# Kernel tuning notes

Hardware: AMD Instinct MI355X
Metric: run time of the kernel (lower is better)

The kernel has to match this reference:

```python
import jax, jax.numpy as jnp
import numpy as np

B, S, D = 1, 2048, 2048
HQ, HKV = 32, 8
HD = D // HQ          # 64
G = HQ // HKV         # 4 query heads per kv head


def apply_rope(x, freq):
    # x: (b, h, s, hd); freq: (s, hd//2) angles. Llama-style pairwise rotation.
    cos = jnp.cos(freq)  # (s, hd//2)
    sin = jnp.sin(freq)
    xr = x.reshape(*x.shape[:-1], HD // 2, 2)
    xe, xo = xr[..., 0], xr[..., 1]
    re = xe * cos - xo * sin
    ro = xe * sin + xo * cos
    return jnp.stack([re, ro], axis=-1).reshape(x.shape)


def setup_inputs() -> dict:
    key = jax.random.key(0)
    k1, k2, k3, k4, k5 = jax.random.split(key, 5)
    x = jax.random.normal(k1, (B, S, D), dtype=jnp.float32)
    # RoPE angles: pos * inv_freq, theta=10000
    inv_freq = 1.0 / (10000.0 ** (jnp.arange(0, HD, 2, dtype=jnp.float32) / HD))
    freq = jnp.arange(S, dtype=jnp.float32)[:, None] * inv_freq[None, :]  # (S, HD//2)
    mask = jnp.tril(jnp.ones((S, S), dtype=jnp.int32))
    scale = D ** -0.5
    wq = jax.random.normal(k2, (D, HQ * HD), dtype=jnp.float32) * scale
    wk = jax.random.normal(k3, (D, HKV * HD), dtype=jnp.float32) * scale
    wv = jax.random.normal(k4, (D, HKV * HD), dtype=jnp.float32) * scale
    wo = jax.random.normal(k5, (HQ * HD, D), dtype=jnp.float32) * scale
    return {"x": x, "freq": freq, "mask": mask, "wq": wq, "wk": wk, "wv": wv, "wo": wo}


def reference(x, freq, mask, wq, wk, wv, wo):
    b, s, d = x.shape
    q = (x @ wq).reshape(b, s, HQ, HD).transpose(0, 2, 1, 3)    # (b,HQ,s,hd)
    k = (x @ wk).reshape(b, s, HKV, HD).transpose(0, 2, 1, 3)   # (b,HKV,s,hd)
    v = (x @ wv).reshape(b, s, HKV, HD).transpose(0, 2, 1, 3)
    q = apply_rope(q, freq[:s])
    k = apply_rope(k, freq[:s])
    # GQA: broadcast kv heads over groups instead of repeat_interleave
    qg = q.reshape(b, HKV, G, s, HD)
    scores = jnp.einsum('bhgsd,bhtd->bhgst', qg, k)             # (b,HKV,G,s,s)
    scores = jnp.where(mask[:s, :s] == 0, -jnp.inf, scores)
    w = jax.nn.softmax(scores * (HD ** -0.5), axis=-1)
    out = jnp.einsum('bhgst,bhtd->bhgsd', w, v)
    out = out.reshape(b, HQ, s, HD).transpose(0, 2, 1, 3).reshape(b, s, HQ * HD)
    return out @ wo
```

## Files before the change

kernel.cpp:

```cpp
#include <hip/hip_runtime.h>

typedef unsigned short u16;
typedef unsigned int u32;
typedef unsigned long long u64;

using bf16x8 = __bf16 __attribute__((ext_vector_type(8)));
using f32x4  = float  __attribute__((ext_vector_type(4)));

#define LDS_SPACE __attribute__((address_space(3)))
#define GLB_SPACE __attribute__((address_space(1)))

static __device__ __forceinline__ u16 f2bf(float f) {
  union { float f; u32 u; } c; c.f = f;
  u32 u = c.u;
  return (u16)((u + 0x7fffu + ((u >> 16) & 1u)) >> 16);
}
static __device__ __forceinline__ float bf2f(u16 u) {
  union { u32 u; float f; } c; c.u = ((u32)u) << 16;
  return c.f;
}

static __device__ __forceinline__ void fence_barrier() {
  asm volatile("" ::: "memory");
  __builtin_amdgcn_s_barrier();
  asm volatile("" ::: "memory");
}

constexpr float SC = 0.18033688011112042f;

__device__ __constant__ unsigned char kItems[40] = {
  12, 28, 29, 42, 44, 45, 46, 57, 59, 60, 61, 62, 63,
  24, 25, 37, 38, 40, 41, 49, 51, 52, 53, 54, 55, 56, 58,
  8, 20, 21, 32, 33, 34, 36, 48, 50,
  16, 17,
  4,
  0
};

__global__ __launch_bounds__(256) void prep_k(const float* __restrict__ x,
                                              const float* __restrict__ wq,
                                              const float* __restrict__ wk,
                                              const float* __restrict__ wv,
                                              const float* __restrict__ wo,
                                              u16* __restrict__ x_bf,
                                              u16* __restrict__ wqkv_t,
                                              u16* __restrict__ wo_t) {
  const int b = blockIdx.x;
  if (b < 4096) {
    int i = b * 256 + threadIdx.x;
    float4 v = ((const float4*)x)[i];
    ushort4 o;
    o.x = f2bf(v.x); o.y = f2bf(v.y); o.z = f2bf(v.z); o.w = f2bf(v.w);
    ((ushort4*)x_bf)[i] = o;
    return;
  }
  const float* src; u16* dst; int C, bx, by; float scale = 1.0f;
  if (b < 8192)      { src = wq; dst = wqkv_t; C = 2048; int t = b - 4096; bx = t & 63; by = t >> 6; scale = SC; }
  else if (b < 9216) { src = wk; dst = wqkv_t + (size_t)2048 * 2048; C = 512; int t = b - 8192; bx = t & 15; by = t >> 4; }
  else if (b < 10240){ src = wv; dst = wqkv_t + (size_t)2560 * 2048; C = 512; int t = b - 9216; bx = t & 15; by = t >> 4; }
  else               { src = wo; dst = wo_t; C = 2048; int t = b - 10240; bx = t & 63; by = t >> 6; }
  __shared__ float t[32][33];
  const int lx = threadIdx.x & 31, ly = threadIdx.x >> 5;
  const int r0 = by * 32, c0 = bx * 32;
  #pragma unroll
  for (int i = 0; i < 32; i += 8)
    t[ly + i][lx] = src[(size_t)(r0 + ly + i) * C + c0 + lx];
  __syncthreads();
  #pragma unroll
  for (int i = 0; i < 32; i += 8)
    dst[(size_t)(c0 + ly + i) * 2048 + r0 + lx] = f2bf(t[lx][ly + i] * scale);
}

__global__ __launch_bounds__(256) void vtrans_k(const u16* __restrict__ Y,
                                                u16* __restrict__ Vt) {
  __shared__ u16 t[64][72];
  const int s0 = blockIdx.x * 64;
  const int c0 = blockIdx.y * 64;
  const int lx = threadIdx.x & 63, ly = threadIdx.x >> 6;
  #pragma unroll
  for (int i = 0; i < 64; i += 4)
    t[i + ly][lx] = Y[(size_t)(s0 + i + ly) * 3072 + 2560 + c0 + lx];
  __syncthreads();
  #pragma unroll
  for (int i = 0; i < 64; i += 4)
    Vt[(size_t)(c0 + i + ly) * 2048 + s0 + lx] = t[lx][i + ly];
}

template <typename OutT, int BN>
__global__ __launch_bounds__(256) void gemm64_k(const u16* __restrict__ A,
                                                const u16* __restrict__ Bt,
                                                OutT* __restrict__ C,
                                                int M, int N, int K) {
  constexpr int WN = BN / 32;
  __shared__ u16 As[2][64 * 64];
  __shared__ u16 Bs[2][BN * 64];
  const int tid = threadIdx.x, lane = tid & 63, w = tid >> 6;
  const int wr = w >> 1, wc = w & 1;
  const int bm = blockIdx.y, bn = blockIdx.x;
  const int l15 = lane & 15, lq = lane >> 4;
  f32x4 acc[2][WN] = {};

  const int srow8 = lane >> 3;
  const int scolb = ((lane & 7) ^ srow8) * 16;
  const u16* AgR = A + (size_t)(bm * 64 + w * 16 + srow8) * K;
  const u16* BgR = Bt + (size_t)(bn * BN + w * (BN / 4) + srow8) * K;

  auto stage = [&](int buf, int k0) {
    #pragma unroll
    for (int i = 0; i < 2; ++i)
      __builtin_amdgcn_global_load_lds(
          (const GLB_SPACE u32*)((const char*)(AgR + (size_t)i * 8 * K + k0) + scolb),
          (LDS_SPACE u32*)&As[buf][(w * 16 + i * 8) * 64], 16, 0, 0);
    #pragma unroll
    for (int i = 0; i < WN; ++i)
      __builtin_amdgcn_global_load_lds(
          (const GLB_SPACE u32*)((const char*)(BgR + (size_t)i * 8 * K + k0) + scolb),
          (LDS_SPACE u32*)&Bs[buf][(w * (BN / 4) + i * 8) * 64], 16, 0, 0);
  };

  stage(0, 0);
  asm volatile("s_waitcnt vmcnt(0)" ::: "memory");
  fence_barrier();

  for (int k0 = 0; k0 < K; k0 += 64) {
    const int p = (k0 >> 6) & 1;
    if (k0 + 64 < K) stage(p ^ 1, k0 + 64);

    #pragma unroll
    for (int kk = 0; kk < 2; ++kk) {
      bf16x8 a[2], b[WN];
      #pragma unroll
      for (int m = 0; m < 2; ++m) {
        const int ra = wr * 32 + m * 16 + l15;
        a[m] = *(const bf16x8*)&As[p][ra * 64 + (((kk * 4 + lq) ^ (ra & 7)) << 3)];
      }
      #pragma unroll
      for (int n = 0; n < WN; ++n) {
        const int rb = wc * (BN / 2) + n * 16 + l15;
        b[n] = *(const bf16x8*)&Bs[p][rb * 64 + (((kk * 4 + lq) ^ (rb & 7)) << 3)];
      }
      #pragma unroll
      for (int m = 0; m < 2; ++m)
        #pragma unroll
        for (int n = 0; n < WN; ++n)
          acc[m][n] = __builtin_amdgcn_mfma_f32_16x16x32_bf16(a[m], b[n], acc[m][n], 0, 0, 0);
    }

    asm volatile("s_waitcnt vmcnt(0)" ::: "memory");
    fence_barrier();
  }

  const int r0 = bm * 64 + wr * 32 + lq * 4;
  const int c0 = bn * BN + wc * (BN / 2) + l15;
  #pragma unroll
  for (int m = 0; m < 2; ++m)
    #pragma unroll
    for (int n = 0; n < WN; ++n)
      #pragma unroll
      for (int r = 0; r < 4; ++r) {
        float v = acc[m][n][r];
        size_t off = (size_t)(r0 + m * 16 + r) * N + (c0 + n * 16);
        if constexpr (sizeof(OutT) == 2) ((u16*)C)[off] = f2bf(v);
        else C[off] = v;
      }
}

__global__ __launch_bounds__(256) void rope_k(u16* __restrict__ Y,
                                              const float* __restrict__ freq) {
  int idx = blockIdx.x * 256 + threadIdx.x;
  int s = idx / 1280;
  int rem = idx - s * 1280;
  int h = rem >> 5;
  int i = rem & 31;
  int col = (h < 32) ? (h * 64 + 2 * i) : (2048 + (h - 32) * 64 + 2 * i);
  float ang = freq[s * 32 + i];
  float sn, cs;
  sincosf(ang, &sn, &cs);
  size_t base = (size_t)s * 3072 + col;
  float e = bf2f(Y[base]), o = bf2f(Y[base + 1]);
  Y[base]     = f2bf(e * cs - o * sn);
  Y[base + 1] = f2bf(e * sn + o * cs);
}

__global__ __launch_bounds__(256, 3) void attn_part_k(const u16* __restrict__ Y,
                                                      const u16* __restrict__ Vtg,
                                                      u16* __restrict__ Opart,
                                                      float2* __restrict__ Ml,
                                                      u16* __restrict__ Out) {
  __shared__ u16 Ks[2][64 * 64];
  __shared__ u16 Vs[2][64 * 64];
  __shared__ u32 Ps[4][16 * 32];
  const int w = threadIdx.x >> 6, lane = threadIdx.x & 63;
  const int l15 = lane & 15, lq = lane >> 4;

  const int b = (int)blockIdx.x;
  const int head = b & 31;
  const int idx = b >> 5;
  const int v = kItems[idx];
  const int qt = v >> 2, ch = v & 3;
  const int kvh = head >> 2;
  const int ntiles = 2 * qt + 2;
  const int nch = qt < 4 ? 1 : qt < 8 ? 2 : qt < 12 ? 3 : 4;
  const int tstart = (ch * ntiles) / nch;
  const int tend = ((ch + 1) * ntiles) / nch;
  const int q0w = qt * 128 + w * 32;

  const int srow = lane >> 3;
  const int scolb = ((lane & 7) ^ srow) * 16;
  const char* gkB = (const char*)(Y + (size_t)(w * 16 + srow) * 3072 + 2048 + kvh * 64) + scolb;
  const char* gvB = (const char*)(Vtg + (size_t)(kvh * 64 + w * 16 + srow) * 2048) + scolb;

  auto stage = [&](int buf, int t) {
    const size_t t0 = (size_t)t * 64;
    #pragma unroll
    for (int i = 0; i < 2; ++i) {
      __builtin_amdgcn_global_load_lds((const GLB_SPACE u32*)(gkB + t0 * 6144 + (size_t)i * 49152),
                                       (LDS_SPACE u32*)&Ks[buf][(w * 16 + i * 8) * 64], 16, 0, 0);
      __builtin_amdgcn_global_load_lds((const GLB_SPACE u32*)(gvB + t0 * 2 + (size_t)i * 32768),
                                       (LDS_SPACE u32*)&Vs[buf][(w * 16 + i * 8) * 64], 16, 0, 0);
    }
  };

  int rowB[4], xk[2], pwr[4], prd[2];
  #pragma unroll
  for (int kt = 0; kt < 4; ++kt) rowB[kt] = (kt * 16 + l15) * 128;
  #pragma unroll
  for (int kk = 0; kk < 2; ++kk) xk[kk] = (((kk * 4 + lq) ^ (l15 & 7)) << 4);
  #pragma unroll
  for (int n = 0; n < 4; ++n)
    pwr[n] = (l15 * 32 + ((lq * 2 + n * 8) ^ ((l15 & 7) << 2))) * 4;
  #pragma unroll
  for (int c = 0; c < 2; ++c)
    prd[c] = l15 * 128 + (((c * 32 + lq * 8) ^ ((l15 & 7) << 3)) << 1);

  bf16x8 qf[2][2];
  #pragma unroll
  for (int qs = 0; qs < 2; ++qs)
    #pragma unroll
    for (int kk = 0; kk < 2; ++kk)
      qf[qs][kk] = *(const bf16x8*)&Y[(size_t)(q0w + qs * 16 + l15) * 3072 +
                                      head * 64 + kk * 32 + lq * 8];

  float m_[2] = { -1e30f, -1e30f };
  float l_[2] = { 0.f, 0.f };
  f32x4 accO[2][4] = {};

  stage(0, tstart);
  asm volatile("s_waitcnt vmcnt(0)" ::: "memory");
  fence_barrier();

  for (int t = tstart; t < tend; ++t) {
    const int p = (t - tstart) & 1;
    stage(p ^ 1, (t + 1 < tend) ? t + 1 : t);

    const int t0 = t * 64;
    if (t0 <= q0w + 31) {
      const char* KbC = (const char*)Ks[p];
      const char* VbC = (const char*)Vs[p];

      f32x4 sc[2][4] = {};
      #pragma unroll
      for (int kk = 0; kk < 2; ++kk)
        #pragma unroll
        for (int kt = 0; kt < 4; ++kt) {
          bf16x8 a = *(const bf16x8*)(KbC + rowB[kt] + xk[kk]);
          sc[0][kt] = __builtin_amdgcn_mfma_f32_16x16x32_bf16(a, qf[0][kk], sc[0][kt], 0, 0, 0);
          sc[1][kt] = __builtin_amdgcn_mfma_f32_16x16x32_bf16(a, qf[1][kk], sc[1][kt], 0, 0, 0);
        }

      bf16x8 vf[2][4];
      #pragma unroll
      for (int c = 0; c < 2; ++c)
        #pragma unroll
        for (int dt = 0; dt < 4; ++dt)
          vf[c][dt] = *(const bf16x8*)(VbC + rowB[dt] + xk[c]);

      #pragma unroll
      for (int qs = 0; qs < 2; ++qs) {
        const int qsmin = q0w + qs * 16;
        if (t0 > qsmin + 15) continue;
        const int qrow = qsmin + l15;
        if (t0 + 63 > qsmin) {
          #pragma unroll
          for (int n = 0; n < 4; ++n)
            #pragma unroll
            for (int rr = 0; rr < 4; ++rr)
              if (t0 + n * 16 + lq * 4 + rr > qrow) sc[qs][n][rr] = -1e30f;
        }
        float a0 = fmaxf(fmaxf(sc[qs][0][0], sc[qs][0][1]), fmaxf(sc[qs][0][2], sc[qs][0][3]));
        float a1 = fmaxf(fmaxf(sc[qs][1][0], sc[qs][1][1]), fmaxf(sc[qs][1][2], sc[qs][1][3]));
        float a2 = fmaxf(fmaxf(sc[qs][2][0], sc[qs][2][1]), fmaxf(sc[qs][2][2], sc[qs][2][3]));
        float a3 = fmaxf(fmaxf(sc[qs][3][0], sc[qs][3][1]), fmaxf(sc[qs][3][2], sc[qs][3][3]));
        float mx = fmaxf(fmaxf(a0, a1), fmaxf(a2, a3));

        if (__any(mx > m_[qs] + 7.25f)) {
          float mf = mx;
          mf = fmaxf(mf, __shfl_xor(mf, 16));
          mf = fmaxf(mf, __shfl_xor(mf, 32));
          const float mnew = fmaxf(m_[qs], mf);
          const float alpha = exp2f(m_[qs] - mnew);
          l_[qs] *= alpha;
          #pragma unroll
          for (int dt = 0; dt < 4; ++dt) accO[qs][dt] *= alpha;
          m_[qs] = mnew;
        }
        const float mS = m_[qs];
        float s0 = 0.f, s1 = 0.f, s2 = 0.f, s3 = 0.f;
        char* psB = (char*)Ps[w];
        #pragma unroll
        for (int n = 0; n < 4; ++n) {
          float p0 = exp2f(sc[qs][n][0] - mS);
          float p1 = exp2f(sc[qs][n][1] - mS);
          float p2 = exp2f(sc[qs][n][2] - mS);
          float p3 = exp2f(sc[qs][n][3] - mS);
          s0 += p0; s1 += p1; s2 += p2; s3 += p3;
          u32 w0, w1;
          asm("v_cvt_pk_bf16_f32 %0, %1, %2" : "=v"(w0) : "v"(p0), "v"(p1));
          asm("v_cvt_pk_bf16_f32 %0, %1, %2" : "=v"(w1) : "v"(p2), "v"(p3));
          *(u64*)(psB + pwr[n]) = (u64)w0 | ((u64)w1 << 32);
        }
        l_[qs] += (s0 + s1) + (s2 + s3);

        #pragma unroll
        for (int c = 0; c < 2; ++c) {
          bf16x8 bb = *(const bf16x8*)(psB + prd[c]);
          #pragma unroll
          for (int dt = 0; dt < 4; ++dt)
            accO[qs][dt] = __builtin_amdgcn_mfma_f32_16x16x32_bf16(vf[c][dt], bb, accO[qs][dt], 0, 0, 0);
        }
      }
    }

    asm volatile("s_waitcnt vmcnt(0)" ::: "memory");
    fence_barrier();
  }

  if (nch == 1) {
    #pragma unroll
    for (int qs = 0; qs < 2; ++qs) {
      float lt = l_[qs];
      lt += __shfl_xor(lt, 16);
      lt += __shfl_xor(lt, 32);
      const float rl = 1.0f / lt;
      const int qrow = q0w + qs * 16 + l15;
      #pragma unroll
      for (int dt = 0; dt < 4; ++dt) {
        ushort4 o;
        o.x = f2bf(accO[qs][dt][0] * rl);
        o.y = f2bf(accO[qs][dt][1] * rl);
        o.z = f2bf(accO[qs][dt][2] * rl);
        o.w = f2bf(accO[qs][dt][3] * rl);
        *(ushort4*)&Out[(size_t)qrow * 2048 + head * 64 + dt * 16 + lq * 4] = o;
      }
    }
    return;
  }

  const int off = qt < 8 ? (qt - 4) * 2 : qt < 12 ? 8 + (qt - 8) * 3 : 20 + (qt - 12) * 4;
  const int slot = head * 36 + off + ch;
  u16* ob = Opart + (size_t)slot * 8192;
  #pragma unroll
  for (int qs = 0; qs < 2; ++qs) {
    float lt = l_[qs];
    lt += __shfl_xor(lt, 16);
    lt += __shfl_xor(lt, 32);
    const int row = w * 32 + qs * 16 + l15;
    #pragma unroll
    for (int dt = 0; dt < 4; ++dt) {
      ushort4 o;
      o.x = f2bf(accO[qs][dt][0]);
      o.y = f2bf(accO[qs][dt][1]);
      o.z = f2bf(accO[qs][dt][2]);
      o.w = f2bf(accO[qs][dt][3]);
      *(ushort4*)&ob[row * 64 + dt * 16 + lq * 4] = o;
    }
    if (lq == 0) Ml[(size_t)slot * 128 + row] = make_float2(m_[qs], lt);
  }
}

__global__ __launch_bounds__(256) void attn_comb_k(const u16* __restrict__ Opart,
                                                   const float2* __restrict__ Ml,
                                                   u16* __restrict__ Out) {
  const int b = blockIdx.x;
  const int rg = b & 3;
  const int hq = b >> 2;
  const int head = hq / 12;
  const int qt = (hq - head * 12) + 4;
  const int nch = qt < 8 ? 2 : qt < 12 ? 3 : 4;
  const int off = qt < 8 ? (qt - 4) * 2 : qt < 12 ? 8 + (qt - 8) * 3 : 20 + (qt - 12) * 4;
  const int slot0 = head * 36 + off;
  const int rl = threadIdx.x >> 3;
  const int d8 = (threadIdx.x & 7) * 8;
  const int row = rg * 32 + rl;

  float gm = -1e30f;
  #pragma unroll 4
  for (int c = 0; c < nch; ++c)
    gm = fmaxf(gm, Ml[(size_t)(slot0 + c) * 128 + row].x);
  float den = 0.f;
  float num[8] = {};
  #pragma unroll 4
  for (int c = 0; c < nch; ++c) {
    float2 ml = Ml[(size_t)(slot0 + c) * 128 + row];
    float a = exp2f(ml.x - gm);
    den += a * ml.y;
    const u16* p = &Opart[(size_t)(slot0 + c) * 8192 + row * 64 + d8];
    ushort4 p0 = *(const ushort4*)p;
    ushort4 p1 = *(const ushort4*)(p + 4);
    num[0] += a * bf2f(p0.x); num[1] += a * bf2f(p0.y);
    num[2] += a * bf2f(p0.z); num[3] += a * bf2f(p0.w);
    num[4] += a * bf2f(p1.x); num[5] += a * bf2f(p1.y);
    num[6] += a * bf2f(p1.z); num[7] += a * bf2f(p1.w);
  }
  const float rd = 1.0f / den;
  ushort4 o0, o1;
  o0.x = f2bf(num[0] * rd); o0.y = f2bf(num[1] * rd);
  o0.z = f2bf(num[2] * rd); o0.w = f2bf(num[3] * rd);
  o1.x = f2bf(num[4] * rd); o1.y = f2bf(num[5] * rd);
  o1.z = f2bf(num[6] * rd); o1.w = f2bf(num[7] * rd);
  u16* op = &Out[(size_t)(qt * 128 + row) * 2048 + head * 64 + d8];
  *(ushort4*)op = o0;
  *(ushort4*)(op + 4) = o1;
}

extern "C" void kernel_launch(void* const* d_in, const int* in_sizes, int n_in,
                              void* d_out, int out_size, void* d_ws, size_t ws_size,
                              hipStream_t stream) {
  const float* x    = (const float*)d_in[0];
  const float* freq = (const float*)d_in[1];
  const float* wq   = (const float*)d_in[3];
  const float* wk   = (const float*)d_in[4];
  const float* wv   = (const float*)d_in[5];
  const float* wo   = (const float*)d_in[6];
  float* out = (float*)d_out;

  u16* x_bf   = (u16*)d_ws;
  u16* wqkv_t = x_bf + (size_t)2048 * 2048;
  u16* wo_t   = wqkv_t + (size_t)3072 * 2048;
  u16* y      = wo_t + (size_t)2048 * 2048;
  u16* attn   = y + (size_t)2048 * 3072;
  u16* vt     = x_bf;
  u16* opart  = attn + (size_t)2048 * 2048;
  float2* ml  = (float2*)(opart + (size_t)1152 * 8192);

  prep_k<<<14336, 256, 0, stream>>>(x, wq, wk, wv, wo, x_bf, wqkv_t, wo_t);
  gemm64_k<u16, 128><<<dim3(24, 32), 256, 0, stream>>>(x_bf, wqkv_t, y, 2048, 3072, 2048);
  rope_k<<<10240, 256, 0, stream>>>(y, freq);
  vtrans_k<<<dim3(32, 8), 256, 0, stream>>>(y, vt);
  attn_part_k<<<1280, 256, 0, stream>>>(y, vt, opart, ml, attn);
  attn_comb_k<<<1536, 256, 0, stream>>>(opart, ml, attn);
  gemm64_k<float, 64><<<dim3(32, 32), 256, 0, stream>>>(attn, wo_t, out, 2048, 2048, 2048);
}
```

Measured before the change: 136.7 us.

## Share K/V tiles across GQA query heads with 512-thread attention blocks

Restructures the split-KV attention kernel so each 512-thread block serves all four query heads of one KV head over a 64-row query band. The K/V tiles are loaded into LDS once for the four heads instead of once per head, and the work list is rebuilt with finer bands and chunks. The combine kernel and the partial-output layout are changed to match. In exchange, the per-tile causal skip is dropped, larger blocks may lower occupancy, and the number of partials to combine changes.

```diff
diff --git a/kernel.cpp b/kernel.cpp
--- a/kernel.cpp
+++ b/kernel.cpp
@@ -28,13 +28,14 @@
 
 constexpr float SC = 0.18033688011112042f;
 
-__device__ __constant__ unsigned char kItems[40] = {
-  12, 28, 29, 42, 44, 45, 46, 57, 59, 60, 61, 62, 63,
-  24, 25, 37, 38, 40, 41, 49, 51, 52, 53, 54, 55, 56, 58,
-  8, 20, 21, 32, 33, 34, 36, 48, 50,
-  16, 17,
-  4,
-  0
+__device__ __constant__ unsigned char kItems8[80] = {
+  124,125,126,127,121,122,123,117,119,115,92,93,94,89,90,86,60,61,57,28,
+  120,116,118,112,113,114,108,109,110,111,105,106,107,101,103,99,88,84,85,80,
+  81,82,77,78,74,56,52,53,49,24,
+  104,100,102,96,97,98,76,72,73,68,69,70,65,66,48,44,45,41,20,
+  64,40,36,37,33,16,
+  32,12,
+  8,4,0
 };
 
 __global__ __launch_bounds__(256) void prep_k(const float* __restrict__ x,
@@ -182,43 +183,40 @@
   Y[base + 1] = f2bf(e * sn + o * cs);
 }
 
-__global__ __launch_bounds__(256, 3) void attn_part_k(const u16* __restrict__ Y,
-                                                      const u16* __restrict__ Vtg,
-                                                      u16* __restrict__ Opart,
-                                                      float2* __restrict__ Ml,
-                                                      u16* __restrict__ Out) {
+__global__ __launch_bounds__(512) void attn_part_k(const u16* __restrict__ Y,
+                                                   const u16* __restrict__ Vtg,
+                                                   u16* __restrict__ Opart,
+                                                   float2* __restrict__ Ml,
+                                                   u16* __restrict__ Out) {
   __shared__ u16 Ks[2][64 * 64];
   __shared__ u16 Vs[2][64 * 64];
-  __shared__ u32 Ps[4][16 * 32];
+  __shared__ u32 Ps[8][16 * 32];
   const int w = threadIdx.x >> 6, lane = threadIdx.x & 63;
   const int l15 = lane & 15, lq = lane >> 4;
 
-  const int b = (int)blockIdx.x;
-  const int head = b & 31;
-  const int idx = b >> 5;
-  const int v = kItems[idx];
-  const int qt = v >> 2, ch = v & 3;
-  const int kvh = head >> 2;
-  const int ntiles = 2 * qt + 2;
-  const int nch = qt < 4 ? 1 : qt < 8 ? 2 : qt < 12 ? 3 : 4;
-  const int tstart = (ch * ntiles) / nch;
-  const int tend = ((ch + 1) * ntiles) / nch;
-  const int q0w = qt * 128 + w * 32;
+  const int kvh = (int)blockIdx.x & 7;
+  const int idx = (int)blockIdx.x >> 3;
+  const int v = kItems8[idx];
+  const int band = v >> 2, ch = v & 3;
+  const int head = kvh * 4 + (w & 3);
+  const int hi = w >> 2;
+  const int n = band + 1;
+  const int nch = (band + 8) >> 3;
+  const int tstart = (ch * n) / nch;
+  const int tend = ((ch + 1) * n) / nch;
+  const int q0w = band * 64 + hi * 32;
 
   const int srow = lane >> 3;
   const int scolb = ((lane & 7) ^ srow) * 16;
-  const char* gkB = (const char*)(Y + (size_t)(w * 16 + srow) * 3072 + 2048 + kvh * 64) + scolb;
-  const char* gvB = (const char*)(Vtg + (size_t)(kvh * 64 + w * 16 + srow) * 2048) + scolb;
+  const char* gkB = (const char*)(Y + (size_t)(w * 8 + srow) * 3072 + 2048 + kvh * 64) + scolb;
+  const char* gvB = (const char*)(Vtg + (size_t)(kvh * 64 + w * 8 + srow) * 2048) + scolb;
 
   auto stage = [&](int buf, int t) {
     const size_t t0 = (size_t)t * 64;
-    #pragma unroll
-    for (int i = 0; i < 2; ++i) {
-      __builtin_amdgcn_global_load_lds((const GLB_SPACE u32*)(gkB + t0 * 6144 + (size_t)i * 49152),
-                                       (LDS_SPACE u32*)&Ks[buf][(w * 16 + i * 8) * 64], 16, 0, 0);
-      __builtin_amdgcn_global_load_lds((const GLB_SPACE u32*)(gvB + t0 * 2 + (size_t)i * 32768),
-                                       (LDS_SPACE u32*)&Vs[buf][(w * 16 + i * 8) * 64], 16, 0, 0);
-    }
+    __builtin_amdgcn_global_load_lds((const GLB_SPACE u32*)(gkB + t0 * 6144),
+                                     (LDS_SPACE u32*)&Ks[buf][(w * 8) * 64], 16, 0, 0);
+    __builtin_amdgcn_global_load_lds((const GLB_SPACE u32*)(gvB + t0 * 2),
+                                     (LDS_SPACE u32*)&Vs[buf][(w * 8) * 64], 16, 0, 0);
   };
 
   int rowB[4], xk[2], pwr[4], prd[2];
@@ -227,8 +225,8 @@
   #pragma unroll
   for (int kk = 0; kk < 2; ++kk) xk[kk] = (((kk * 4 + lq) ^ (l15 & 7)) << 4);
   #pragma unroll
-  for (int n = 0; n < 4; ++n)
-    pwr[n] = (l15 * 32 + ((lq * 2 + n * 8) ^ ((l15 & 7) << 2))) * 4;
+  for (int nn = 0; nn < 4; ++nn)
+    pwr[nn] = (l15 * 32 + ((lq * 2 + nn * 8) ^ ((l15 & 7) << 2))) * 4;
   #pragma unroll
   for (int c = 0; c < 2; ++c)
     prd[c] = l15 * 128 + (((c * 32 + lq * 8) ^ ((l15 & 7) << 3)) << 1);
@@ -254,7 +252,7 @@
     stage(p ^ 1, (t + 1 < tend) ? t + 1 : t);
 
     const int t0 = t * 64;
-    if (t0 <= q0w + 31) {
+    {
       const char* KbC = (const char*)Ks[p];
       const char* VbC = (const char*)Vs[p];
 
@@ -282,10 +280,10 @@
         const int qrow = qsmin + l15;
         if (t0 + 63 > qsmin) {
           #pragma unroll
-          for (int n = 0; n < 4; ++n)
+          for (int nn = 0; nn < 4; ++nn)
             #pragma unroll
             for (int rr = 0; rr < 4; ++rr)
-              if (t0 + n * 16 + lq * 4 + rr > qrow) sc[qs][n][rr] = -1e30f;
+              if (t0 + nn * 16 + lq * 4 + rr > qrow) sc[qs][nn][rr] = -1e30f;
         }
         float a0 = fmaxf(fmaxf(sc[qs][0][0], sc[qs][0][1]), fmaxf(sc[qs][0][2], sc[qs][0][3]));
         float a1 = fmaxf(fmaxf(sc[qs][1][0], sc[qs][1][1]), fmaxf(sc[qs][1][2], sc[qs][1][3]));
@@ -308,16 +306,16 @@
         float s0 = 0.f, s1 = 0.f, s2 = 0.f, s3 = 0.f;
         char* psB = (char*)Ps[w];
         #pragma unroll
-        for (int n = 0; n < 4; ++n) {
-          float p0 = exp2f(sc[qs][n][0] - mS);
-          float p1 = exp2f(sc[qs][n][1] - mS);
-          float p2 = exp2f(sc[qs][n][2] - mS);
-          float p3 = exp2f(sc[qs][n][3] - mS);
+        for (int nn = 0; nn < 4; ++nn) {
+          float p0 = exp2f(sc[qs][nn][0] - mS);
+          float p1 = exp2f(sc[qs][nn][1] - mS);
+          float p2 = exp2f(sc[qs][nn][2] - mS);
+          float p3 = exp2f(sc[qs][nn][3] - mS);
           s0 += p0; s1 += p1; s2 += p2; s3 += p3;
           u32 w0, w1;
           asm("v_cvt_pk_bf16_f32 %0, %1, %2" : "=v"(w0) : "v"(p0), "v"(p1));
           asm("v_cvt_pk_bf16_f32 %0, %1, %2" : "=v"(w1) : "v"(p2), "v"(p3));
-          *(u64*)(psB + pwr[n]) = (u64)w0 | ((u64)w1 << 32);
+          *(u64*)(psB + pwr[nn]) = (u64)w0 | ((u64)w1 << 32);
         }
         l_[qs] += (s0 + s1) + (s2 + s3);
 
@@ -356,15 +354,15 @@
     return;
   }
 
-  const int off = qt < 8 ? (qt - 4) * 2 : qt < 12 ? 8 + (qt - 8) * 3 : 20 + (qt - 12) * 4;
-  const int slot = head * 36 + off + ch;
-  u16* ob = Opart + (size_t)slot * 8192;
+  const int g = 2 * band + hi;
+  const int slot = (head * 48 + (g - 16)) * 4 + ch;
+  u16* ob = Opart + (size_t)slot * 2048;
   #pragma unroll
   for (int qs = 0; qs < 2; ++qs) {
     float lt = l_[qs];
     lt += __shfl_xor(lt, 16);
     lt += __shfl_xor(lt, 32);
-    const int row = w * 32 + qs * 16 + l15;
+    const int row = qs * 16 + l15;
     #pragma unroll
     for (int dt = 0; dt < 4; ++dt) {
       ushort4 o;
@@ -374,7 +372,7 @@
       o.w = f2bf(accO[qs][dt][3]);
       *(ushort4*)&ob[row * 64 + dt * 16 + lq * 4] = o;
     }
-    if (lq == 0) Ml[(size_t)slot * 128 + row] = make_float2(m_[qs], lt);
+    if (lq == 0) Ml[(size_t)slot * 32 + row] = make_float2(m_[qs], lt);
   }
 }
 
@@ -382,29 +380,27 @@
                                                    const float2* __restrict__ Ml,
                                                    u16* __restrict__ Out) {
   const int b = blockIdx.x;
-  const int rg = b & 3;
-  const int hq = b >> 2;
-  const int head = hq / 12;
-  const int qt = (hq - head * 12) + 4;
-  const int nch = qt < 8 ? 2 : qt < 12 ? 3 : 4;
-  const int off = qt < 8 ? (qt - 4) * 2 : qt < 12 ? 8 + (qt - 8) * 3 : 20 + (qt - 12) * 4;
-  const int slot0 = head * 36 + off;
+  const int head = b / 48;
+  const int gi = b - head * 48;
+  const int g = gi + 16;
+  const int band = g >> 1;
+  const int nch = (band + 8) >> 3;
+  const int slot0 = b * 4;
   const int rl = threadIdx.x >> 3;
   const int d8 = (threadIdx.x & 7) * 8;
-  const int row = rg * 32 + rl;
 
   float gm = -1e30f;
   #pragma unroll 4
   for (int c = 0; c < nch; ++c)
-    gm = fmaxf(gm, Ml[(size_t)(slot0 + c) * 128 + row].x);
+    gm = fmaxf(gm, Ml[(size_t)(slot0 + c) * 32 + rl].x);
   float den = 0.f;
   float num[8] = {};
   #pragma unroll 4
   for (int c = 0; c < nch; ++c) {
-    float2 ml = Ml[(size_t)(slot0 + c) * 128 + row];
+    float2 ml = Ml[(size_t)(slot0 + c) * 32 + rl];
     float a = exp2f(ml.x - gm);
     den += a * ml.y;
-    const u16* p = &Opart[(size_t)(slot0 + c) * 8192 + row * 64 + d8];
+    const u16* p = &Opart[(size_t)(slot0 + c) * 2048 + rl * 64 + d8];
     ushort4 p0 = *(const ushort4*)p;
     ushort4 p1 = *(const ushort4*)(p + 4);
     num[0] += a * bf2f(p0.x); num[1] += a * bf2f(p0.y);
@@ -418,7 +414,7 @@
   o0.z = f2bf(num[2] * rd); o0.w = f2bf(num[3] * rd);
   o1.x = f2bf(num[4] * rd); o1.y = f2bf(num[5] * rd);
   o1.z = f2bf(num[6] * rd); o1.w = f2bf(num[7] * rd);
-  u16* op = &Out[(size_t)(qt * 128 + row) * 2048 + head * 64 + d8];
+  u16* op = &Out[(size_t)(g * 32 + rl) * 2048 + head * 64 + d8];
   *(ushort4*)op = o0;
   *(ushort4*)(op + 4) = o1;
 }
@@ -441,13 +437,13 @@
   u16* attn   = y + (size_t)2048 * 3072;
   u16* vt     = x_bf;
   u16* opart  = attn + (size_t)2048 * 2048;
-  float2* ml  = (float2*)(opart + (size_t)1152 * 8192);
+  float2* ml  = (float2*)(opart + (size_t)6144 * 2048);
 
   prep_k<<<14336, 256, 0, stream>>>(x, wq, wk, wv, wo, x_bf, wqkv_t, wo_t);
   gemm64_k<u16, 128><<<dim3(24, 32), 256, 0, stream>>>(x_bf, wqkv_t, y, 2048, 3072, 2048);
   rope_k<<<10240, 256, 0, stream>>>(y, freq);
   vtrans_k<<<dim3(32, 8), 256, 0, stream>>>(y, vt);
-  attn_part_k<<<1280, 256, 0, stream>>>(y, vt, opart, ml, attn);
+  attn_part_k<<<640, 512, 0, stream>>>(y, vt, opart, ml, attn);
   attn_comb_k<<<1536, 256, 0, stream>>>(opart, ml, attn);
   gemm64_k<float, 64><<<dim3(32, 32), 256, 0, stream>>>(attn, wo_t, out, 2048, 2048, 2048);
 }
```

New measurement: 152.1 us. 11.3% more time.

## Replace double-buffered KV prefetch with synchronous 128-key superstage loads

Applied to the files above, without the earlier changes.

The attention loop used to prefetch the next 64-key tile into the second LDS buffer while computing on the current one. It now loads two 64-key tiles (128 keys) into both buffers at once, waits for them, computes both, and barriers. This halves the number of barriers and loop iterations. In exchange it gives up the overlap of global loads with MFMA compute, so load latency is exposed on every superstage unless occupancy hides it. Chunk boundaries are now set in 128-key units.

```diff
diff --git a/kernel.cpp b/kernel.cpp
--- a/kernel.cpp
+++ b/kernel.cpp
@@ -199,10 +199,10 @@
   const int v = kItems[idx];
   const int qt = v >> 2, ch = v & 3;
   const int kvh = head >> 2;
-  const int ntiles = 2 * qt + 2;
+  const int nst = qt + 1;
   const int nch = qt < 4 ? 1 : qt < 8 ? 2 : qt < 12 ? 3 : 4;
-  const int tstart = (ch * ntiles) / nch;
-  const int tend = ((ch + 1) * ntiles) / nch;
+  const int sstart = (ch * nst) / nch;
+  const int send = ((ch + 1) * nst) / nch;
   const int q0w = qt * 128 + w * 32;
 
   const int srow = lane >> 3;
@@ -210,14 +210,17 @@
   const char* gkB = (const char*)(Y + (size_t)(w * 16 + srow) * 3072 + 2048 + kvh * 64) + scolb;
   const char* gvB = (const char*)(Vtg + (size_t)(kvh * 64 + w * 16 + srow) * 2048) + scolb;
 
-  auto stage = [&](int buf, int t) {
-    const size_t t0 = (size_t)t * 64;
-    #pragma unroll
-    for (int i = 0; i < 2; ++i) {
-      __builtin_amdgcn_global_load_lds((const GLB_SPACE u32*)(gkB + t0 * 6144 + (size_t)i * 49152),
-                                       (LDS_SPACE u32*)&Ks[buf][(w * 16 + i * 8) * 64], 16, 0, 0);
-      __builtin_amdgcn_global_load_lds((const GLB_SPACE u32*)(gvB + t0 * 2 + (size_t)i * 32768),
-                                       (LDS_SPACE u32*)&Vs[buf][(w * 16 + i * 8) * 64], 16, 0, 0);
+  auto stage = [&](int st) {
+    #pragma unroll
+    for (int h = 0; h < 2; ++h) {
+      const size_t t0 = (size_t)st * 128 + h * 64;
+      #pragma unroll
+      for (int i = 0; i < 2; ++i) {
+        __builtin_amdgcn_global_load_lds((const GLB_SPACE u32*)(gkB + t0 * 6144 + (size_t)i * 49152),
+                                         (LDS_SPACE u32*)&Ks[h][(w * 16 + i * 8) * 64], 16, 0, 0);
+        __builtin_amdgcn_global_load_lds((const GLB_SPACE u32*)(gvB + t0 * 2 + (size_t)i * 32768),
+                                         (LDS_SPACE u32*)&Vs[h][(w * 16 + i * 8) * 64], 16, 0, 0);
+      }
     }
   };
 
@@ -245,18 +248,17 @@
   float l_[2] = { 0.f, 0.f };
   f32x4 accO[2][4] = {};
 
-  stage(0, tstart);
-  asm volatile("s_waitcnt vmcnt(0)" ::: "memory");
-  fence_barrier();
-
-  for (int t = tstart; t < tend; ++t) {
-    const int p = (t - tstart) & 1;
-    stage(p ^ 1, (t + 1 < tend) ? t + 1 : t);
-
-    const int t0 = t * 64;
-    if (t0 <= q0w + 31) {
-      const char* KbC = (const char*)Ks[p];
-      const char* VbC = (const char*)Vs[p];
+  for (int st = sstart; st < send; ++st) {
+    stage(st);
+    asm volatile("s_waitcnt vmcnt(0)" ::: "memory");
+    fence_barrier();
+
+    #pragma unroll
+    for (int h = 0; h < 2; ++h) {
+      const int t0 = st * 128 + h * 64;
+      if (t0 > q0w + 31) continue;
+      const char* KbC = (const char*)Ks[h];
+      const char* VbC = (const char*)Vs[h];
 
       f32x4 sc[2][4] = {};
       #pragma unroll
@@ -331,7 +333,6 @@
       }
     }
 
-    asm volatile("s_waitcnt vmcnt(0)" ::: "memory");
     fence_barrier();
   }
 
```

Result: no change. 137.4 us (+0.6%).
